# Kernel optimization log

Hardware: AMD Instinct MI355X
Metric: run time of the kernel (lower is better)

The kernel has to match this reference:

```python
import jax, jax.numpy as jnp
import numpy as np

K = 8          # opt.pk, explicit precision cutoff
MARGIN = 0.2   # opt.margin
NEG = -1e30    # sentinel for masked sort keys


def setup_inputs() -> dict:
    key = jax.random.key(0)
    k1, k2 = jax.random.split(key)
    batch_reprs = jax.random.normal(k1, (4096, 512), dtype=jnp.float32)
    batch_labels = jax.random.randint(k2, (4096,), 0, 64)
    return {"batch_reprs": batch_reprs, "batch_labels": batch_labels}


def _forward(batch_reprs, batch_labels):
    B = batch_reprs.shape[0]
    dt = batch_reprs.dtype
    # cls_match_mat: 1 if same class
    match = (batch_labels[:, None] == batch_labels[None, :]).astype(dt)
    # pairwise euclidean distance (squared=False), safe sqrt at zero diagonal
    sq = jnp.sum(batch_reprs * batch_reprs, axis=1)
    res = jnp.maximum(sq[:, None] - 2.0 * (batch_reprs @ batch_reprs.T) + sq[None, :], 0.0)
    zero = res <= 0.0
    d = jnp.where(zero, 0.0, jnp.sqrt(jnp.where(zero, 1.0, res)))
    sim_hat = -d + (1.0 - match) * MARGIN  # use_margin=True path
    # rank via double argsort (descending similarity -> rank 1 = best)
    order = jnp.argsort(-sim_hat, axis=1)
    rank = jnp.argsort(order, axis=1).astype(dt) + 1.0
    pos_nums = jnp.sum(match, axis=1)
    ks = jnp.minimum(pos_nums, jnp.asarray(K + 1, dt))[:, None]  # k_mat per row
    w = 1.0 / jnp.log2(rank + 1.0) + 1.0  # DCG-style rank weight
    # false positives: not same class, within top-k_i
    fp_mask = (match < 1.0) & (rank <= ks)
    fp_nums = jnp.sum(fp_mask, axis=1)  # |N| per row
    # false negatives: same class, beyond top-k_i
    fn_mask = (match > 0.0) & (rank > ks)
    fp_term = jnp.sum(jnp.where(fp_mask, sim_hat * w, 0.0))
    # per-row variable-size topk over false negatives, vectorized:
    # mask non-FN entries to -inf, sort desc, keep first fp_nums[i] entries
    fn_key = jnp.where(fn_mask, sim_hat, NEG)
    fn_order = jnp.argsort(-fn_key, axis=1)
    sorted_sim = jnp.take_along_axis(sim_hat, fn_order, axis=1)
    sorted_w = jnp.take_along_axis(w, fn_order, axis=1)
    sorted_valid = jnp.take_along_axis(fn_mask, fn_order, axis=1)
    take = (jnp.arange(B)[None, :].astype(dt) < fp_nums[:, None]) & sorted_valid
    fn_term = jnp.sum(jnp.where(take, sorted_sim * sorted_w, 0.0))
    # rows with fp_num==0 contribute 0 to both terms, matching the host loop
    return fp_term - fn_term


def reference(batch_reprs, batch_labels):
    return _forward(batch_reprs, batch_labels)
```

## Files before the change

kernel.cpp:

```cpp
#include <hip/hip_runtime.h>
#include <math.h>

#define BB 4096
#define DD 512
#define KTOP 9
#define MARGIN_F 0.2f
#define NT 32
#define NTRI (NT * (NT + 1) / 2)

typedef __attribute__((ext_vector_type(8))) short short8;
typedef __attribute__((ext_vector_type(4))) float f32x4;
typedef unsigned long long u64;

__device__ unsigned short g_Rhi[(size_t)BB * DD];
__device__ u64 g_cmask[64 * 64];

__device__ __forceinline__ unsigned short f2bf(float x) {
  unsigned u = __float_as_uint(x);
  u += 0x7fffu + ((u >> 16) & 1u);
  return (unsigned short)(u >> 16);
}

__device__ __forceinline__ void gload16(void* lds, const void* g) {
  __builtin_amdgcn_global_load_lds(
      (const __attribute__((address_space(1))) void*)g,
      (__attribute__((address_space(3))) void*)lds, 16, 0, 0);
}

__device__ __forceinline__ float ord16val(unsigned o16) {
  unsigned e = (o16 << 16) | 0x8000u;
  unsigned s = (e & 0x80000000u) ? (e ^ 0x80000000u) : ~e;
  return __uint_as_float(s);
}

__device__ __forceinline__ unsigned wavemax32_dpp(unsigned c) {
#define MSTEP(CTRL, RM)                                                        \
  {                                                                            \
    unsigned o = (unsigned)__builtin_amdgcn_update_dpp(0, (int)c, CTRL, RM, 0xf, false); \
    if (o > c) c = o;                                                          \
  }
  MSTEP(0xB1, 0xf) MSTEP(0x4E, 0xf) MSTEP(0x141, 0xf) MSTEP(0x140, 0xf)
  MSTEP(0x142, 0xa) MSTEP(0x143, 0xc)
#undef MSTEP
  return (unsigned)__builtin_amdgcn_readlane((int)c, 63);
}

__device__ __forceinline__ int wavesum_dpp(int c) {
#define SSTEP(CTRL, RM)                                                        \
  c += __builtin_amdgcn_update_dpp(0, c, CTRL, RM, 0xf, false);
  SSTEP(0xB1, 0xf) SSTEP(0x4E, 0xf) SSTEP(0x141, 0xf) SSTEP(0x140, 0xf)
  SSTEP(0x142, 0xa) SSTEP(0x143, 0xc)
#undef SSTEP
  return __builtin_amdgcn_readlane(c, 63);
}

__device__ __forceinline__ unsigned u4c(const uint4& f, int q) {
  return q == 0 ? f.x : q == 1 ? f.y : q == 2 ? f.z : f.w;
}

__global__ __launch_bounds__(64) void splitsq(const float* __restrict__ R,
                                              float* __restrict__ sq) {
  const int row = blockIdx.x, lane = threadIdx.x;
  const float4* r4 = (const float4*)(R + (size_t)row * DD);
  float4 a = r4[lane], b = r4[lane + 64];
  float xs[8] = {a.x, a.y, a.z, a.w, b.x, b.y, b.z, b.w};
  unsigned short hs[8];
  float s = 0.f;
  #pragma unroll
  for (int q = 0; q < 8; ++q) {
    float x = xs[q];
    s += x * x;
    hs[q] = f2bf(x);
  }
  const size_t base = (size_t)row * DD;
  *(ushort4*)&g_Rhi[base + lane * 4]       = *(ushort4*)&hs[0];
  *(ushort4*)&g_Rhi[base + 256 + lane * 4] = *(ushort4*)&hs[4];
  #pragma unroll
  for (int off = 32; off; off >>= 1) s += __shfl_down(s, off);
  if (lane == 0) sq[row] = s;
}

__global__ __launch_bounds__(64) void buildmask(const int* __restrict__ labels) {
  __shared__ int slab[BB];
  const int c = blockIdx.x, lane = threadIdx.x;
  for (int i = lane; i < BB / 4; i += 64) ((int4*)slab)[i] = ((const int4*)labels)[i];
  __syncthreads();
  u64 m = 0;
  #pragma unroll
  for (int e = 0; e < 64; ++e) {
    int j = 512 * (e >> 3) + 8 * lane + (e & 7);
    m |= (u64)(slab[j] == c) << e;
  }
  g_cmask[c * 64 + lane] = m;
}

__global__ __launch_bounds__(256) void simgemm_sb(const int* __restrict__ labels,
                                                  const float* __restrict__ sq,
                                                  unsigned short* __restrict__ simq) {
  const int x = blockIdx.x & 7;
  int c = blockIdx.x >> 3;
  int bi = 0, bj = 0;
  #pragma unroll
  for (int q = 0; q < 4; ++q) {
    const int bjq = (q < 2) ? (2 * x + q) : (28 - 2 * x + q);
    const int n = bjq + 1;
    if (c >= 0 && c < n) { bj = bjq; bi = c; }
    c -= n;
  }
  const int i0 = bi * 128, j0 = bj * 128;

  __shared__ __align__(16) unsigned char smembytes[35840];
  unsigned short (*kbuf)[8192] = (unsigned short (*)[8192])smembytes;

  const int tid = threadIdx.x;
  const int wid = tid >> 6, lane = tid & 63;
  const int wr = wid >> 1, wc = wid & 1;
  const int lrow = lane & 15, kblk = lane >> 4;

  f32x4 acc[4][4] = {};

  auto stage = [&](int k0) {
    const int sr = lane & 15;
    const int sc = (lane >> 4) * 8;
    #pragma unroll
    for (int i = 0; i < 2; ++i) {
      const int chunk = 2 * wid + i;
      const int r = chunk * 16 + sr;
      #pragma unroll
      for (int s = 0; s < 2; ++s) {
        gload16(&kbuf[0][chunk * 1024 + s * 512],
                &g_Rhi[(size_t)(i0 + r) * DD + k0 + s * 32 + sc]);
        gload16(&kbuf[1][chunk * 1024 + s * 512],
                &g_Rhi[(size_t)(j0 + r) * DD + k0 + s * 32 + sc]);
      }
    }
  };

  for (int step = 0; step < 8; ++step) {
    if (step) __syncthreads();
    stage(step * 64);
    __syncthreads();

    #pragma unroll
    for (int kk = 0; kk < 2; ++kk) {
      short8 a[4], b[4];
      #pragma unroll
      for (int m = 0; m < 4; ++m)
        a[m] = *(const short8*)&kbuf[0][(wr * 4 + m) * 1024 + kk * 512 + lane * 8];
      #pragma unroll
      for (int n = 0; n < 4; ++n)
        b[n] = *(const short8*)&kbuf[1][(wc * 4 + n) * 1024 + kk * 512 + lane * 8];
      #pragma unroll
      for (int m = 0; m < 4; ++m) {
        #pragma unroll
        for (int n = 0; n < 4; ++n) {
          acc[m][n] = __builtin_amdgcn_mfma_f32_16x16x32_bf16(a[m], b[n], acc[m][n], 0, 0, 0);
        }
      }
    }
  }

  __syncthreads();
  unsigned short (*T)[132] = (unsigned short (*)[132])smembytes;
  float* sqi = (float*)(smembytes + 33792);
  float* sqj = (float*)(smembytes + 34304);
  int* labi  = (int*)(smembytes + 34816);
  int* labj  = (int*)(smembytes + 35328);
  if (tid < 128) { sqi[tid] = sq[i0 + tid]; labi[tid] = labels[i0 + tid]; }
  else { int t2 = tid - 128; sqj[t2] = sq[j0 + t2]; labj[t2] = labels[j0 + t2]; }
  __syncthreads();

  #pragma unroll
  for (int m = 0; m < 4; ++m) {
    const int rbase = wr * 64 + m * 16 + kblk * 4;
    #pragma unroll
    for (int n = 0; n < 4; ++n) {
      const int ccol = wc * 64 + n * 16 + lrow;
      const float sqc = sqj[ccol];
      const int lc_ = labj[ccol];
      #pragma unroll
      for (int reg = 0; reg < 4; ++reg) {
        const int r = rbase + reg;
        float res = sqi[r] - 2.0f * acc[m][n][reg] + sqc;
        float dd = (res <= 0.f) ? 0.f : sqrtf(res);
        float sv = -dd + ((labi[r] != lc_) ? MARGIN_F : 0.f);
        unsigned su = __float_as_uint(sv);
        unsigned ord = su ^ ((unsigned)((int)su >> 31) | 0x80000000u);
        T[r][ccol] = (unsigned short)(ord >> 16);
      }
    }
  }
  __syncthreads();

  const int srow0 = tid >> 4, scol0 = (tid & 15) * 8;
  #pragma unroll
  for (int p = 0; p < 8; ++p) {
    const int r = p * 16 + srow0;
    short8 w = *(const short8*)&T[r][scol0];
    *(short8*)&simq[(size_t)(i0 + r) * BB + j0 + scol0] = w;
  }
  if (bi != bj) {
    #pragma unroll
    for (int p = 0; p < 8; ++p) {
      const int col = p * 16 + srow0;
      unsigned short tmp[8];
      #pragma unroll
      for (int t = 0; t < 8; ++t) tmp[t] = T[scol0 + t][col];
      *(short8*)&simq[(size_t)(j0 + col) * BB + i0 + scol0] = *(short8*)tmp;
    }
  }
}

#define TOP2UPD(k, a, b) {                                                     \
  unsigned _mx = ((k) > (a)) ? (k) : (a);                                      \
  unsigned _mn = ((k) > (a)) ? (a) : (k);                                      \
  (a) = _mx;                                                                   \
  (b) = (_mn > (b)) ? _mn : (b); }

__global__ __launch_bounds__(256) void rowproc7(const unsigned short* __restrict__ simq,
                                                const int* __restrict__ labels,
                                                float* __restrict__ partials) {
  const int tid = threadIdx.x;
  const int lane = tid & 63;
  const int row = blockIdx.x * 4 + (tid >> 6);

  const int myl = labels[row];
  const u64 mask = g_cmask[myl * 64 + lane];
  const unsigned lbase2 = (unsigned)((4095 - 8 * lane) << 1);

  const uint4* rowp = (const uint4*)(simq + (size_t)row * BB);
  unsigned k[64];
  #pragma unroll
  for (int s = 0; s < 8; ++s) {
    uint4 w = rowp[lane + s * 64];
    const unsigned base_s = lbase2 - (unsigned)(1024 * s);
    #pragma unroll
    for (int q = 0; q < 4; ++q) {
      const unsigned wv = u4c(w, q);
      const int e0 = s * 8 + q * 2;
      k[e0]     = ((wv & 0xffffu) << 13)
                | (base_s - (unsigned)((q * 2) << 1)     + (unsigned)((mask >> e0) & 1ull));
      k[e0 + 1] = ((wv >> 16) << 13)
                | (base_s - (unsigned)((q * 2 + 1) << 1) + (unsigned)((mask >> (e0 + 1)) & 1ull));
    }
  }

  unsigned h1 = 0, h2 = 0;
  #pragma unroll
  for (int e = 0; e < 64; ++e) TOP2UPD(k[e], h1, h2);
  const int pos = wavesum_dpp(__popcll(mask));
  const int ks = min(pos, KTOP);

  unsigned kth = 0;
  float fp = 0.f; int fpn = 0;
  #pragma unroll
  for (int t = 0; t < KTOP; ++t) {
    if (t < ks) {
      unsigned g = wavemax32_dpp(h1);
      if (!(g & 1u)) { fp += ord16val(g >> 13) * (1.f / log2f((float)(t + 2)) + 1.f); fpn++; }
      if (t == ks - 1) kth = g;
      if (h1 == g) {
        h1 = h2; h2 = ~0u;
        if (h1 == ~0u) {
          h1 = 0; h2 = 0;
          #pragma unroll
          for (int e = 0; e < 64; ++e) {
            if (k[e] < g) TOP2UPD(k[e], h1, h2);
          }
        }
      }
    }
  }

  float fn = 0.f;
  if (fpn > 0) {
    unsigned f1 = 0, f2 = 0;
    #pragma unroll
    for (int e = 0; e < 64; ++e) {
      if ((k[e] & 1u) && k[e] < kth) TOP2UPD(k[e], f1, f2);
    }
    unsigned ck[KTOP];
    int nc = 0;
    #pragma unroll
    for (int u = 0; u < KTOP; ++u) {
      ck[u] = ~0u;
      if (u < fpn) {
        unsigned g = wavemax32_dpp(f1);
        if (g != 0u) {
          ck[u] = g; nc = u + 1;
          if (f1 == g) {
            f1 = f2; f2 = ~0u;
            if (f1 == ~0u) {
              f1 = 0; f2 = 0;
              #pragma unroll
              for (int e = 0; e < 64; ++e) {
                if ((k[e] & 1u) && k[e] < g) TOP2UPD(k[e], f1, f2);
              }
            }
          }
        }
      }
    }
    if (nc > 0) {
      int cnt[KTOP];
      #pragma unroll
      for (int u = 0; u < KTOP; ++u) cnt[u] = 0;
      #pragma unroll
      for (int e = 0; e < 64; ++e) {
        #pragma unroll
        for (int u = 0; u < KTOP; ++u) cnt[u] += (k[e] > ck[u]) ? 1 : 0;
      }
      #pragma unroll
      for (int u = 0; u < KTOP; ++u) cnt[u] = wavesum_dpp(cnt[u]);
      #pragma unroll
      for (int u = 0; u < KTOP; ++u) {
        if (u < nc) {
          int rank = 1 + cnt[u];
          fn += ord16val(ck[u] >> 13) * (1.f / log2f((float)(rank + 1)) + 1.f);
        }
      }
    }
  }

  if (lane == 0) partials[row] = fp - fn;
}

__global__ __launch_bounds__(256) void finalreduce(const float* __restrict__ partials,
                                                   float* __restrict__ out) {
  __shared__ float s[256];
  const int tid = threadIdx.x;
  float acc = 0.f;
  for (int j = tid; j < BB; j += 256) acc += partials[j];
  s[tid] = acc; __syncthreads();
  #pragma unroll
  for (int st = 128; st; st >>= 1) { if (tid < st) s[tid] += s[tid + st]; __syncthreads(); }
  if (tid == 0) out[0] = s[0];
}

extern "C" void kernel_launch(void* const* d_in, const int* in_sizes, int n_in,
                              void* d_out, int out_size, void* d_ws, size_t ws_size,
                              hipStream_t stream) {
  const float* R      = (const float*)d_in[0];
  const int*   labels = (const int*)d_in[1];
  float* out = (float*)d_out;

  unsigned short* simq = (unsigned short*)d_ws;
  float* sq            = (float*)((char*)d_ws + (size_t)BB * BB * 2);
  float* partials      = sq + BB;

  splitsq<<<BB, 64, 0, stream>>>(R, sq);
  buildmask<<<64, 64, 0, stream>>>(labels);
  simgemm_sb<<<NTRI, 256, 0, stream>>>(labels, sq, simq);
  rowproc7<<<BB / 4, 256, 0, stream>>>(simq, labels, partials);
  finalreduce<<<1, 256, 0, stream>>>(partials, out);
}
```

Measured before the change: 99.34 us.

## Double-buffer GEMM tiles via register prefetch instead of direct global-to-LDS loads

Replaces the single-buffered global_load_lds staging in the similarity GEMM with a register-staged double buffer. The next k-slice is loaded into registers while MFMAs run on the current LDS buffer, then written to the alternate buffer, so only one barrier per step is needed. The aim is to hide global load latency behind compute. In exchange, LDS use grows to 64KB and register pressure rises, which may reduce occupancy.

Measured after the change: 127.0 us. 1.28x slower.

```diff
diff --git a/kernel.cpp b/kernel.cpp
--- a/kernel.cpp
+++ b/kernel.cpp
@@ -19,12 +19,6 @@
   unsigned u = __float_as_uint(x);
   u += 0x7fffu + ((u >> 16) & 1u);
   return (unsigned short)(u >> 16);
-}
-
-__device__ __forceinline__ void gload16(void* lds, const void* g) {
-  __builtin_amdgcn_global_load_lds(
-      (const __attribute__((address_space(1))) void*)g,
-      (__attribute__((address_space(3))) void*)lds, 16, 0, 0);
 }
 
 __device__ __forceinline__ float ord16val(unsigned o16) {
@@ -94,7 +88,7 @@
   g_cmask[c * 64 + lane] = m;
 }
 
-__global__ __launch_bounds__(256) void simgemm_sb(const int* __restrict__ labels,
+__global__ __launch_bounds__(256) void simgemm_rs(const int* __restrict__ labels,
                                                   const float* __restrict__ sq,
                                                   unsigned short* __restrict__ simq) {
   const int x = blockIdx.x & 7;
@@ -109,47 +103,61 @@
   }
   const int i0 = bi * 128, j0 = bj * 128;
 
-  __shared__ __align__(16) unsigned char smembytes[35840];
-  unsigned short (*kbuf)[8192] = (unsigned short (*)[8192])smembytes;
+  __shared__ __align__(16) unsigned char smembytes[65536];
+  unsigned short (*kbuf)[2][8192] = (unsigned short (*)[2][8192])smembytes;
 
   const int tid = threadIdx.x;
   const int wid = tid >> 6, lane = tid & 63;
   const int wr = wid >> 1, wc = wid & 1;
   const int lrow = lane & 15, kblk = lane >> 4;
 
+  const int sr = lane & 15;
+  const int sc = (lane >> 4) * 8;
+
   f32x4 acc[4][4] = {};
-
-  auto stage = [&](int k0) {
-    const int sr = lane & 15;
-    const int sc = (lane >> 4) * 8;
+  uint4 rg[8];
+
+  auto stage_load = [&](int k0) {
+    #pragma unroll
+    for (int i = 0; i < 2; ++i) {
+      const int r = (2 * wid + i) * 16 + sr;
+      #pragma unroll
+      for (int s = 0; s < 2; ++s) {
+        rg[i * 4 + s * 2 + 0] = *(const uint4*)&g_Rhi[(size_t)(i0 + r) * DD + k0 + s * 32 + sc];
+        rg[i * 4 + s * 2 + 1] = *(const uint4*)&g_Rhi[(size_t)(j0 + r) * DD + k0 + s * 32 + sc];
+      }
+    }
+  };
+  auto stage_write = [&](int buf) {
+    const int loff = lane * 8;
     #pragma unroll
     for (int i = 0; i < 2; ++i) {
       const int chunk = 2 * wid + i;
-      const int r = chunk * 16 + sr;
       #pragma unroll
       for (int s = 0; s < 2; ++s) {
-        gload16(&kbuf[0][chunk * 1024 + s * 512],
-                &g_Rhi[(size_t)(i0 + r) * DD + k0 + s * 32 + sc]);
-        gload16(&kbuf[1][chunk * 1024 + s * 512],
-                &g_Rhi[(size_t)(j0 + r) * DD + k0 + s * 32 + sc]);
+        *(uint4*)&kbuf[buf][0][chunk * 1024 + s * 512 + loff] = rg[i * 4 + s * 2 + 0];
+        *(uint4*)&kbuf[buf][1][chunk * 1024 + s * 512 + loff] = rg[i * 4 + s * 2 + 1];
       }
     }
   };
 
+  stage_load(0);
+  stage_write(0);
+  stage_load(64);
+  __syncthreads();
+
   for (int step = 0; step < 8; ++step) {
-    if (step) __syncthreads();
-    stage(step * 64);
-    __syncthreads();
+    const int cur = step & 1;
 
     #pragma unroll
     for (int kk = 0; kk < 2; ++kk) {
       short8 a[4], b[4];
       #pragma unroll
       for (int m = 0; m < 4; ++m)
-        a[m] = *(const short8*)&kbuf[0][(wr * 4 + m) * 1024 + kk * 512 + lane * 8];
+        a[m] = *(const short8*)&kbuf[cur][0][(wr * 4 + m) * 1024 + kk * 512 + lane * 8];
       #pragma unroll
       for (int n = 0; n < 4; ++n)
-        b[n] = *(const short8*)&kbuf[1][(wc * 4 + n) * 1024 + kk * 512 + lane * 8];
+        b[n] = *(const short8*)&kbuf[cur][1][(wc * 4 + n) * 1024 + kk * 512 + lane * 8];
       #pragma unroll
       for (int m = 0; m < 4; ++m) {
         #pragma unroll
@@ -157,6 +165,12 @@
           acc[m][n] = __builtin_amdgcn_mfma_f32_16x16x32_bf16(a[m], b[n], acc[m][n], 0, 0, 0);
         }
       }
+    }
+
+    if (step < 7) {
+      stage_write(cur ^ 1);
+      if (step < 6) stage_load((step + 2) * 64);
+      __syncthreads();
     }
   }
 
@@ -350,7 +364,7 @@
 
   splitsq<<<BB, 64, 0, stream>>>(R, sq);
   buildmask<<<64, 64, 0, stream>>>(labels);
-  simgemm_sb<<<NTRI, 256, 0, stream>>>(labels, sq, simq);
+  simgemm_rs<<<NTRI, 256, 0, stream>>>(labels, sq, simq);
   rowproc7<<<BB / 4, 256, 0, stream>>>(simq, labels, partials);
   finalreduce<<<1, 256, 0, stream>>>(partials, out);
 }
```

## Switch similarity GEMM to full-grid 256x256 tiles with double-buffered LDS

Applied to the files above, without the earlier changes.

Replaces the symmetric upper-triangle 128x128 tile GEMM, which wrote each off-diagonal tile twice with a transpose, with a full 16x16 grid of 256x256 tiles using 512 threads. The K loop now double-buffers LDS loads, prefetching the next 32-wide slice while computing the current one. The aim is more data reuse per tile and overlap of global loads with MFMA work. In exchange it computes the whole matrix instead of half, roughly doubling the MFMA work, and it writes the epilogue out in four serialized quarter passes.

After: 104.1 us. +4.8%, slower.

```diff
diff --git a/kernel.cpp b/kernel.cpp
--- a/kernel.cpp
+++ b/kernel.cpp
@@ -5,8 +5,6 @@
 #define DD 512
 #define KTOP 9
 #define MARGIN_F 0.2f
-#define NT 32
-#define NTRI (NT * (NT + 1) / 2)
 
 typedef __attribute__((ext_vector_type(8))) short short8;
 typedef __attribute__((ext_vector_type(4))) float f32x4;
@@ -94,120 +92,109 @@
   g_cmask[c * 64 + lane] = m;
 }
 
-__global__ __launch_bounds__(256) void simgemm_sb(const int* __restrict__ labels,
-                                                  const float* __restrict__ sq,
-                                                  unsigned short* __restrict__ simq) {
+__global__ __launch_bounds__(512, 2) void simgemm_256(const int* __restrict__ labels,
+                                                      const float* __restrict__ sq,
+                                                      unsigned short* __restrict__ simq) {
   const int x = blockIdx.x & 7;
-  int c = blockIdx.x >> 3;
-  int bi = 0, bj = 0;
-  #pragma unroll
-  for (int q = 0; q < 4; ++q) {
-    const int bjq = (q < 2) ? (2 * x + q) : (28 - 2 * x + q);
-    const int n = bjq + 1;
-    if (c >= 0 && c < n) { bj = bjq; bi = c; }
-    c -= n;
-  }
-  const int i0 = bi * 128, j0 = bj * 128;
-
-  __shared__ __align__(16) unsigned char smembytes[35840];
-  unsigned short (*kbuf)[8192] = (unsigned short (*)[8192])smembytes;
+  const int c = blockIdx.x >> 3;
+  const int bj = 2 * x + (c >> 4);
+  const int bi = c & 15;
+  const int i0 = bi * 256, j0 = bj * 256;
+
+  __shared__ __align__(16) unsigned char smembytes[65536];
+  unsigned short (*kbufA)[8192] = (unsigned short (*)[8192])smembytes;
+  unsigned short (*kbufB)[8192] = (unsigned short (*)[8192])(smembytes + 32768);
 
   const int tid = threadIdx.x;
   const int wid = tid >> 6, lane = tid & 63;
-  const int wr = wid >> 1, wc = wid & 1;
+  const int wr = wid >> 2, wc = wid & 3;
   const int lrow = lane & 15, kblk = lane >> 4;
 
-  f32x4 acc[4][4] = {};
-
-  auto stage = [&](int k0) {
-    const int sr = lane & 15;
-    const int sc = (lane >> 4) * 8;
+  const int srow = lane & 15;
+  const int scol = (lane >> 4) * 8;
+
+  f32x4 acc[8][4] = {};
+
+  auto stage = [&](int buf, int k0) {
     #pragma unroll
     for (int i = 0; i < 2; ++i) {
       const int chunk = 2 * wid + i;
-      const int r = chunk * 16 + sr;
-      #pragma unroll
-      for (int s = 0; s < 2; ++s) {
-        gload16(&kbuf[0][chunk * 1024 + s * 512],
-                &g_Rhi[(size_t)(i0 + r) * DD + k0 + s * 32 + sc]);
-        gload16(&kbuf[1][chunk * 1024 + s * 512],
-                &g_Rhi[(size_t)(j0 + r) * DD + k0 + s * 32 + sc]);
-      }
+      const int r = chunk * 16 + srow;
+      gload16(&kbufA[buf][chunk * 512], &g_Rhi[(size_t)(i0 + r) * DD + k0 + scol]);
+      gload16(&kbufB[buf][chunk * 512], &g_Rhi[(size_t)(j0 + r) * DD + k0 + scol]);
     }
   };
 
-  for (int step = 0; step < 8; ++step) {
-    if (step) __syncthreads();
-    stage(step * 64);
+  stage(0, 0);
+
+  for (int step = 0; step < 16; ++step) {
+    const int cur = step & 1;
     __syncthreads();
-
-    #pragma unroll
-    for (int kk = 0; kk < 2; ++kk) {
-      short8 a[4], b[4];
-      #pragma unroll
-      for (int m = 0; m < 4; ++m)
-        a[m] = *(const short8*)&kbuf[0][(wr * 4 + m) * 1024 + kk * 512 + lane * 8];
-      #pragma unroll
-      for (int n = 0; n < 4; ++n)
-        b[n] = *(const short8*)&kbuf[1][(wc * 4 + n) * 1024 + kk * 512 + lane * 8];
-      #pragma unroll
-      for (int m = 0; m < 4; ++m) {
+    if (step < 15) stage(cur ^ 1, (step + 1) * 32);
+
+    short8 a[8], b[4];
+    #pragma unroll
+    for (int m = 0; m < 8; ++m)
+      a[m] = *(const short8*)&kbufA[cur][(wr * 8 + m) * 512 + lane * 8];
+    #pragma unroll
+    for (int n = 0; n < 4; ++n)
+      b[n] = *(const short8*)&kbufB[cur][(wc * 4 + n) * 512 + lane * 8];
+
+    #pragma unroll
+    for (int m = 0; m < 8; ++m) {
+      #pragma unroll
+      for (int n = 0; n < 4; ++n) {
+        acc[m][n] = __builtin_amdgcn_mfma_f32_16x16x32_bf16(a[m], b[n], acc[m][n], 0, 0, 0);
+      }
+    }
+  }
+
+  __syncthreads();
+  unsigned short (*T)[260] = (unsigned short (*)[260])smembytes;
+  float* sqi = (float*)(smembytes + 33280);
+  float* sqj = (float*)(smembytes + 34304);
+  int* labi  = (int*)(smembytes + 35328);
+  int* labj  = (int*)(smembytes + 36352);
+  if (tid < 256) { sqi[tid] = sq[i0 + tid]; labi[tid] = labels[i0 + tid]; }
+  else { int t2 = tid - 256; sqj[t2] = sq[j0 + t2]; labj[t2] = labels[j0 + t2]; }
+  __syncthreads();
+
+  #pragma unroll
+  for (int p = 0; p < 4; ++p) {
+    if (wr == (p >> 1)) {
+      const int mbase = (p & 1) * 4;
+      #pragma unroll
+      for (int mm = 0; mm < 4; ++mm) {
+        const int m = mbase + mm;
+        const int rloc = mm * 16 + kblk * 4;
+        const int rglob = p * 64 + rloc;
         #pragma unroll
         for (int n = 0; n < 4; ++n) {
-          acc[m][n] = __builtin_amdgcn_mfma_f32_16x16x32_bf16(a[m], b[n], acc[m][n], 0, 0, 0);
+          const int ccol = wc * 64 + n * 16 + lrow;
+          const float sqc = sqj[ccol];
+          const int lc_ = labj[ccol];
+          #pragma unroll
+          for (int reg = 0; reg < 4; ++reg) {
+            float res = sqi[rglob + reg] - 2.0f * acc[m][n][reg] + sqc;
+            float dd = (res <= 0.f) ? 0.f : sqrtf(res);
+            float sv = -dd + ((labi[rglob + reg] != lc_) ? MARGIN_F : 0.f);
+            unsigned su = __float_as_uint(sv);
+            unsigned ord = su ^ ((unsigned)((int)su >> 31) | 0x80000000u);
+            T[rloc + reg][ccol] = (unsigned short)(ord >> 16);
+          }
         }
       }
     }
-  }
-
-  __syncthreads();
-  unsigned short (*T)[132] = (unsigned short (*)[132])smembytes;
-  float* sqi = (float*)(smembytes + 33792);
-  float* sqj = (float*)(smembytes + 34304);
-  int* labi  = (int*)(smembytes + 34816);
-  int* labj  = (int*)(smembytes + 35328);
-  if (tid < 128) { sqi[tid] = sq[i0 + tid]; labi[tid] = labels[i0 + tid]; }
-  else { int t2 = tid - 128; sqj[t2] = sq[j0 + t2]; labj[t2] = labels[j0 + t2]; }
-  __syncthreads();
-
-  #pragma unroll
-  for (int m = 0; m < 4; ++m) {
-    const int rbase = wr * 64 + m * 16 + kblk * 4;
-    #pragma unroll
-    for (int n = 0; n < 4; ++n) {
-      const int ccol = wc * 64 + n * 16 + lrow;
-      const float sqc = sqj[ccol];
-      const int lc_ = labj[ccol];
-      #pragma unroll
-      for (int reg = 0; reg < 4; ++reg) {
-        const int r = rbase + reg;
-        float res = sqi[r] - 2.0f * acc[m][n][reg] + sqc;
-        float dd = (res <= 0.f) ? 0.f : sqrtf(res);
-        float sv = -dd + ((labi[r] != lc_) ? MARGIN_F : 0.f);
-        unsigned su = __float_as_uint(sv);
-        unsigned ord = su ^ ((unsigned)((int)su >> 31) | 0x80000000u);
-        T[r][ccol] = (unsigned short)(ord >> 16);
-      }
-    }
-  }
-  __syncthreads();
-
-  const int srow0 = tid >> 4, scol0 = (tid & 15) * 8;
-  #pragma unroll
-  for (int p = 0; p < 8; ++p) {
-    const int r = p * 16 + srow0;
-    short8 w = *(const short8*)&T[r][scol0];
-    *(short8*)&simq[(size_t)(i0 + r) * BB + j0 + scol0] = w;
-  }
-  if (bi != bj) {
-    #pragma unroll
-    for (int p = 0; p < 8; ++p) {
-      const int col = p * 16 + srow0;
-      unsigned short tmp[8];
-      #pragma unroll
-      for (int t = 0; t < 8; ++t) tmp[t] = T[scol0 + t][col];
-      *(short8*)&simq[(size_t)(j0 + col) * BB + i0 + scol0] = *(short8*)tmp;
-    }
+    __syncthreads();
+    {
+      const int rr = tid >> 3, cs = (tid & 7) * 32;
+      unsigned short* dst = &simq[(size_t)(i0 + p * 64 + rr) * BB + j0 + cs];
+      #pragma unroll
+      for (int q2 = 0; q2 < 4; ++q2) {
+        *(short8*)(dst + q2 * 8) = *(const short8*)&T[rr][cs + q2 * 8];
+      }
+    }
+    __syncthreads();
   }
 }
 
@@ -350,7 +337,7 @@
 
   splitsq<<<BB, 64, 0, stream>>>(R, sq);
   buildmask<<<64, 64, 0, stream>>>(labels);
-  simgemm_sb<<<NTRI, 256, 0, stream>>>(labels, sq, simq);
+  simgemm_256<<<256, 512, 0, stream>>>(labels, sq, simq);
   rowproc7<<<BB / 4, 256, 0, stream>>>(simq, labels, partials);
   finalreduce<<<1, 256, 0, stream>>>(partials, out);
 }
```
